# Optimization experiments

Measured on AMD Instinct MI355X. Metric: run time of the kernel, lower is better.

Reference implementation:

```python
import jax, jax.numpy as jnp
import numpy as np

N_NODES = 100000
N_EDGES = 1600000
N_GRAPHS = 250
F_NODE = 9
F_GLOB = 4
H = 64


def _lin(key, fan_out, fan_in):
    s = 1.0 / np.sqrt(fan_in)
    return jax.random.uniform(key, (fan_out, fan_in), jnp.float32, -s, s)


def setup_inputs() -> dict:
    key = jax.random.key(0)
    ks = jax.random.split(key, 24)
    inp = {
        "node_h": jax.random.normal(ks[0], (N_NODES, F_NODE), jnp.float32),
        "x_global_features": jax.random.normal(ks[1], (N_GRAPHS, F_GLOB), jnp.float32),
        "edge_index": jax.random.randint(ks[2], (2, N_EDGES), 0, N_NODES, jnp.int32),
        "batch_idx": jnp.sort(jax.random.randint(ks[3], (N_NODES,), 0, N_GRAPHS, jnp.int32)),
    }
    # SAGEConv params: lin_l (neighbor, with bias) and lin_r (root, no bias)
    dims = [(H, F_NODE + F_GLOB), (H, H), (H, H)]
    k = 4
    for i, (o, fi) in enumerate(dims):
        inp[f"sage{i}_Wl"] = _lin(ks[k], o, fi); k += 1
        inp[f"sage{i}_bl"] = jnp.zeros((o,), jnp.float32)
        inp[f"sage{i}_Wr"] = _lin(ks[k], o, fi); k += 1
    # MLP: 64->64->64->64->1
    mdims = [(H, H), (H, H), (H, H), (1, H)]
    for i, (o, fi) in enumerate(mdims):
        inp[f"mlp_W{i}"] = _lin(ks[k], o, fi); k += 1
        inp[f"mlp_b{i}"] = jnp.zeros((o,), jnp.float32)
    return inp


def _sage_conv(x, src, dst, Wl, bl, Wr):
    # mean aggregation of source features at destination nodes
    msg = x[src]                                             # [E, F]
    agg = jax.ops.segment_sum(msg, dst, num_segments=N_NODES)
    deg = jax.ops.segment_sum(jnp.ones((src.shape[0], 1), x.dtype), dst, num_segments=N_NODES)
    agg = agg / jnp.maximum(deg, 1.0)
    return agg @ Wl.T + bl + x @ Wr.T


def reference(node_h, x_global_features, edge_index, batch_idx,
              sage0_Wl, sage0_bl, sage0_Wr,
              sage1_Wl, sage1_bl, sage1_Wr,
              sage2_Wl, sage2_bl, sage2_Wr,
              mlp_W0, mlp_b0, mlp_W1, mlp_b1, mlp_W2, mlp_b2, mlp_W3, mlp_b3):
    src, dst = edge_index[0], edge_index[1]
    # concat per-node features with gathered global features
    x = jnp.concatenate([node_h, x_global_features[batch_idx]], axis=1)  # [N, 13]
    x = jax.nn.relu(_sage_conv(x, src, dst, sage0_Wl, sage0_bl, sage0_Wr))
    x = jax.nn.relu(_sage_conv(x, src, dst, sage1_Wl, sage1_bl, sage1_Wr))
    x = _sage_conv(x, src, dst, sage2_Wl, sage2_bl, sage2_Wr)            # [N, 64]
    # scatter_mean pooling over graphs
    summed = jax.ops.segment_sum(x, batch_idx, num_segments=N_GRAPHS)
    cnt = jax.ops.segment_sum(jnp.ones((x.shape[0], 1), x.dtype), batch_idx, num_segments=N_GRAPHS)
    pooled = summed / jnp.maximum(cnt, 1.0)                              # [G, 64]
    h = jax.nn.relu(pooled @ mlp_W0.T + mlp_b0)
    h = jax.nn.relu(h @ mlp_W1.T + mlp_b1)
    h = jax.nn.relu(h @ mlp_W2.T + mlp_b2)
    out = h @ mlp_W3.T + mlp_b3                                          # [G, 1]
    return out.reshape(-1)
```

## Files before the change

### kernel.cpp

```cpp
#include <hip/hip_runtime.h>
#include <hip/hip_bf16.h>

#define N_NODES 100000
#define N_EDGES 1600000
#define N_GRAPHS 250
#define NB 391
#define BCAP 6144
#define BIN_BLOCKS 250
#define EPB 6400

typedef __hip_bfloat16 bf16;

__device__ __forceinline__ void atomAddF(float* p, float v) {
  unsafeAtomicAdd(p, v);
}

__device__ __forceinline__ float b2f(unsigned short u) {
  union { unsigned int i; float f; } v; v.i = ((unsigned)u) << 16; return v.f;
}

__device__ __forceinline__ void accb(float4& a, ushort4 u) {
  a.x += b2f(u.x); a.y += b2f(u.y); a.z += b2f(u.z); a.w += b2f(u.w);
}

__device__ __forceinline__ float4 b2f4(ushort4 u) {
  return make_float4(b2f(u.x), b2f(u.y), b2f(u.z), b2f(u.w));
}

__device__ __forceinline__ float4 add4(float4 a, float4 b) {
  return make_float4(a.x + b.x, a.y + b.y, a.z + b.z, a.w + b.w);
}

__global__ void concat_kernel(const float* __restrict__ nh, const float* __restrict__ xg,
                              const int* __restrict__ batch, bf16* __restrict__ x0b) {
  int idx = blockIdx.x * blockDim.x + threadIdx.x;
  if (idx >= N_NODES * 16) return;
  int n = idx >> 4, j = idx & 15;
  float v;
  if (j < 9)       v = nh[n * 9 + j];
  else if (j < 13) v = xg[batch[n] * 4 + (j - 9)];
  else             v = 0.0f;
  x0b[idx] = __float2bfloat16(v);
}

__global__ __launch_bounds__(256) void bin_kernel(const int* __restrict__ src,
                                                  const int* __restrict__ dst,
                                                  int* __restrict__ gcnt,
                                                  int* __restrict__ binned) {
  __shared__ int hist[NB];
  __shared__ int base[NB];
  const int t = threadIdx.x;
  for (int i = t; i < NB; i += 256) hist[i] = 0;
  __syncthreads();
  const int e0 = blockIdx.x * EPB;
  int d[25];
#pragma unroll
  for (int k = 0; k < 25; ++k) {
    d[k] = dst[e0 + k * 256 + t];
    atomicAdd(&hist[d[k] >> 8], 1);
  }
  __syncthreads();
  for (int i = t; i < NB; i += 256) {
    base[i] = atomicAdd(&gcnt[i], hist[i]);
    hist[i] = 0;
  }
  __syncthreads();
#pragma unroll
  for (int k = 0; k < 25; ++k) {
    const int dd = d[k];
    const int b = dd >> 8;
    const int s = src[e0 + k * 256 + t];
    const int r = atomicAdd(&hist[b], 1);
    const int pos = base[b] + r;
    if (pos < BCAP) binned[b * BCAP + pos] = ((dd & 255) << 17) | s;
  }
}

__global__ __launch_bounds__(512) void bucketscan_kernel(const int* __restrict__ gcnt,
                                                         int* __restrict__ bbase,
                                                         int* __restrict__ rowptr) {
  __shared__ int sh[512];
  int t = threadIdx.x;
  int v = (t < NB) ? gcnt[t] : 0;
  sh[t] = v;
  __syncthreads();
  for (int off = 1; off < 512; off <<= 1) {
    int u = (t >= off) ? sh[t - off] : 0;
    __syncthreads();
    sh[t] += u;
    __syncthreads();
  }
  if (t < NB) bbase[t] = sh[t] - v;
  if (t == 0) rowptr[N_NODES] = N_EDGES;
}

__global__ __launch_bounds__(256) void sort_kernel(const int* __restrict__ gcnt,
                                                   const int* __restrict__ bbase,
                                                   const int* __restrict__ binned,
                                                   int* __restrict__ esorted,
                                                   int* __restrict__ rowptr,
                                                   float* __restrict__ inv) {
  __shared__ int cnt[256];
  __shared__ int cur[256];
  __shared__ int sh[256];
  const int b = blockIdx.x, t = threadIdx.x;
  const int count = min(gcnt[b], BCAP);
  const int ebase = bbase[b];
  const int* __restrict__ bin = binned + b * BCAP;
  cnt[t] = 0;
  __syncthreads();
  for (int i = t; i < count; i += 256) atomicAdd(&cnt[bin[i] >> 17], 1);
  __syncthreads();
  const int c = cnt[t];
  sh[t] = c;
  __syncthreads();
  for (int off = 1; off < 256; off <<= 1) {
    int u = (t >= off) ? sh[t - off] : 0;
    __syncthreads();
    sh[t] += u;
    __syncthreads();
  }
  const int p = sh[t] - c;
  cur[t] = p;
  const int node = b * 256 + t;
  if (node < N_NODES) {
    rowptr[node] = ebase + p;
    inv[node] = 1.0f / fmaxf((float)c, 1.0f);
  }
  __syncthreads();
  for (int i = t; i < count; i += 256) {
    const int v = bin[i];
    const int r = atomicAdd(&cur[v >> 17], 1);
    esorted[ebase + r] = v & 0x1FFFF;
  }
}

template <int F, bool RELU, bool OUTF32>
__launch_bounds__(512)
__global__ void sage_fused(const bf16* __restrict__ xb, const int* __restrict__ rowptr,
                           const int* __restrict__ esorted, const float* __restrict__ inv,
                           const float* __restrict__ Wl, const float* __restrict__ bl,
                           const float* __restrict__ Wr, int Fw,
                           float* __restrict__ outf, bf16* __restrict__ outb) {
  constexpr int ST = (F == 64) ? 64 : 20;
  constexpr int NT = 32;
  __shared__ float Wlt[F * 64];
  __shared__ float Wrt[F * 64];
  __shared__ float asld[NT * ST];
  __shared__ float xsld[NT * ST];
  for (int i = threadIdx.x; i < 64 * F; i += 512) {
    int h = i & 63, f = i >> 6;
    Wlt[f * 64 + h] = (f < Fw) ? Wl[h * Fw + f] : 0.0f;
    Wrt[f * 64 + h] = (f < Fw) ? Wr[h * Fw + f] : 0.0f;
  }
  __syncthreads();
  const int lane = threadIdx.x & 63;
  const int w = threadIdx.x >> 6;
  const int q = lane >> 4;
  const int c = lane & 15;
  const int slot = w * 4 + q;
  const float blv = bl[lane];
  const ushort4* xbu = (const ushort4*)xb;
  const int ntiles = N_NODES / NT;
  for (int tile = blockIdx.x; tile < ntiles; tile += gridDim.x) {
    const int n = tile * NT + slot;
    const int e0 = rowptr[n], e1 = rowptr[n + 1];
    const float invn = inv[n];
    if (F == 64) {
      float4 a0 = {0, 0, 0, 0}, a1 = a0, a2 = a0, a3 = a0;
      int e = e0;
      for (; e + 8 <= e1; e += 8) {
        int s0 = esorted[e], s1 = esorted[e + 1], s2 = esorted[e + 2], s3 = esorted[e + 3];
        int s4 = esorted[e + 4], s5 = esorted[e + 5], s6 = esorted[e + 6], s7 = esorted[e + 7];
        ushort4 u0 = xbu[(size_t)s0 * 16 + c];
        ushort4 u1 = xbu[(size_t)s1 * 16 + c];
        ushort4 u2 = xbu[(size_t)s2 * 16 + c];
        ushort4 u3 = xbu[(size_t)s3 * 16 + c];
        ushort4 u4 = xbu[(size_t)s4 * 16 + c];
        ushort4 u5 = xbu[(size_t)s5 * 16 + c];
        ushort4 u6 = xbu[(size_t)s6 * 16 + c];
        ushort4 u7 = xbu[(size_t)s7 * 16 + c];
        accb(a0, u0); accb(a1, u1); accb(a2, u2); accb(a3, u3);
        accb(a0, u4); accb(a1, u5); accb(a2, u6); accb(a3, u7);
      }
      for (; e + 4 <= e1; e += 4) {
        int s0 = esorted[e], s1 = esorted[e + 1], s2 = esorted[e + 2], s3 = esorted[e + 3];
        ushort4 u0 = xbu[(size_t)s0 * 16 + c];
        ushort4 u1 = xbu[(size_t)s1 * 16 + c];
        ushort4 u2 = xbu[(size_t)s2 * 16 + c];
        ushort4 u3 = xbu[(size_t)s3 * 16 + c];
        accb(a0, u0); accb(a1, u1); accb(a2, u2); accb(a3, u3);
      }
      for (; e < e1; ++e) accb(a0, xbu[(size_t)esorted[e] * 16 + c]);
      a0 = add4(add4(a0, a1), add4(a2, a3));
      float4 xv = b2f4(xbu[(size_t)n * 16 + c]);
      a0.x *= invn; a0.y *= invn; a0.z *= invn; a0.w *= invn;
      *(float4*)&asld[slot * ST + 4 * c] = a0;
      *(float4*)&xsld[slot * ST + 4 * c] = xv;
    } else {
      const int eg = c >> 2, cc = c & 3;
      float4 a0 = {0, 0, 0, 0}, a1 = a0;
      int e = e0 + eg;
      for (; e + 4 < e1; e += 8) {
        int sa = esorted[e], sb = esorted[e + 4];
        ushort4 ua = xbu[(size_t)sa * 4 + cc];
        ushort4 ub = xbu[(size_t)sb * 4 + cc];
        accb(a0, ua); accb(a1, ub);
      }
      if (e < e1) accb(a0, xbu[(size_t)esorted[e] * 4 + cc]);
      a0 = add4(a0, a1);
      a0.x += __shfl_xor(a0.x, 4); a0.y += __shfl_xor(a0.y, 4);
      a0.z += __shfl_xor(a0.z, 4); a0.w += __shfl_xor(a0.w, 4);
      a0.x += __shfl_xor(a0.x, 8); a0.y += __shfl_xor(a0.y, 8);
      a0.z += __shfl_xor(a0.z, 8); a0.w += __shfl_xor(a0.w, 8);
      if (eg == 0) {
        float4 xv = b2f4(xbu[(size_t)n * 4 + cc]);
        a0.x *= invn; a0.y *= invn; a0.z *= invn; a0.w *= invn;
        *(float4*)&asld[slot * ST + 4 * cc] = a0;
        *(float4*)&xsld[slot * ST + 4 * cc] = xv;
      }
    }
    __builtin_amdgcn_wave_barrier();
    const float* ar0 = &asld[(w * 4 + 0) * ST];
    const float* ar1 = &asld[(w * 4 + 1) * ST];
    const float* ar2 = &asld[(w * 4 + 2) * ST];
    const float* ar3 = &asld[(w * 4 + 3) * ST];
    const float* xr0 = &xsld[(w * 4 + 0) * ST];
    const float* xr1 = &xsld[(w * 4 + 1) * ST];
    const float* xr2 = &xsld[(w * 4 + 2) * ST];
    const float* xr3 = &xsld[(w * 4 + 3) * ST];
    float o0 = blv, o1 = blv, o2 = blv, o3 = blv;
#pragma unroll
    for (int f = 0; f < F; ++f) {
      float wl = Wlt[f * 64 + lane];
      float wr = Wrt[f * 64 + lane];
      o0 = fmaf(ar0[f], wl, fmaf(xr0[f], wr, o0));
      o1 = fmaf(ar1[f], wl, fmaf(xr1[f], wr, o1));
      o2 = fmaf(ar2[f], wl, fmaf(xr2[f], wr, o2));
      o3 = fmaf(ar3[f], wl, fmaf(xr3[f], wr, o3));
    }
    if (RELU) {
      o0 = fmaxf(o0, 0.0f); o1 = fmaxf(o1, 0.0f);
      o2 = fmaxf(o2, 0.0f); o3 = fmaxf(o3, 0.0f);
    }
    const size_t nb = (size_t)(tile * NT + w * 4) * 64;
    if (OUTF32) {
      outf[nb + lane]       = o0;
      outf[nb + 64 + lane]  = o1;
      outf[nb + 128 + lane] = o2;
      outf[nb + 192 + lane] = o3;
    } else {
      outb[nb + lane]       = __float2bfloat16(o0);
      outb[nb + 64 + lane]  = __float2bfloat16(o1);
      outb[nb + 128 + lane] = __float2bfloat16(o2);
      outb[nb + 192 + lane] = __float2bfloat16(o3);
    }
    __builtin_amdgcn_wave_barrier();
  }
}

__global__ void pool_kernel(const float* __restrict__ x, const int* __restrict__ batch,
                            float* __restrict__ pooled, float* __restrict__ cnt) {
  int wave = (blockIdx.x * blockDim.x + threadIdx.x) >> 6;
  int lane = threadIdx.x & 63;
  int n0 = wave * 64;
  if (n0 >= N_NODES) return;
  int nend = n0 + 64 < N_NODES ? n0 + 64 : N_NODES;
  int cur = -1;
  float acc = 0.0f, run = 0.0f;
  for (int n = n0; n < nend; ++n) {
    int b = batch[n];
    float v = x[(size_t)n * 64 + lane];
    if (b != cur) {
      if (cur >= 0) {
        atomAddF(&pooled[cur * 64 + lane], acc);
        if (lane == 0) atomAddF(&cnt[cur], run);
      }
      cur = b; acc = v; run = 1.0f;
    } else {
      acc += v; run += 1.0f;
    }
  }
  if (cur >= 0) {
    atomAddF(&pooled[cur * 64 + lane], acc);
    if (lane == 0) atomAddF(&cnt[cur], run);
  }
}

__global__ void mlp_kernel(const float* __restrict__ pooled, const float* __restrict__ cnt,
                           const float* __restrict__ W0, const float* __restrict__ b0,
                           const float* __restrict__ W1, const float* __restrict__ b1,
                           const float* __restrict__ W2, const float* __restrict__ b2,
                           const float* __restrict__ W3, const float* __restrict__ b3,
                           float* __restrict__ out) {
  int g = blockIdx.x, t = threadIdx.x;
  __shared__ float buf[2][64];
  float ic = 1.0f / fmaxf(cnt[g], 1.0f);
  buf[0][t] = pooled[g * 64 + t] * ic;
  __syncthreads();
  const float* Ws[3] = {W0, W1, W2};
  const float* Bs[3] = {b0, b1, b2};
  int cur = 0;
  for (int L = 0; L < 3; ++L) {
    const float* W = Ws[L];
    float acc = Bs[L][t];
#pragma unroll
    for (int f = 0; f < 64; ++f) acc = fmaf(W[t * 64 + f], buf[cur][f], acc);
    buf[cur ^ 1][t] = fmaxf(acc, 0.0f);
    __syncthreads();
    cur ^= 1;
  }
  float v = W3[t] * buf[cur][t];
  for (int off = 32; off; off >>= 1) v += __shfl_down(v, off);
  if (t == 0) out[g] = v + b3[0];
}

extern "C" void kernel_launch(void* const* d_in, const int* in_sizes, int n_in,
                              void* d_out, int out_size, void* d_ws, size_t ws_size,
                              hipStream_t stream) {
  const float* nh    = (const float*)d_in[0];
  const float* xg    = (const float*)d_in[1];
  const int*   ei    = (const int*)d_in[2];
  const int*   batch = (const int*)d_in[3];
  const float* s0Wl  = (const float*)d_in[4];
  const float* s0bl  = (const float*)d_in[5];
  const float* s0Wr  = (const float*)d_in[6];
  const float* s1Wl  = (const float*)d_in[7];
  const float* s1bl  = (const float*)d_in[8];
  const float* s1Wr  = (const float*)d_in[9];
  const float* s2Wl  = (const float*)d_in[10];
  const float* s2bl  = (const float*)d_in[11];
  const float* s2Wr  = (const float*)d_in[12];
  const float* mW0   = (const float*)d_in[13];
  const float* mb0   = (const float*)d_in[14];
  const float* mW1   = (const float*)d_in[15];
  const float* mb1   = (const float*)d_in[16];
  const float* mW2   = (const float*)d_in[17];
  const float* mb2   = (const float*)d_in[18];
  const float* mW3   = (const float*)d_in[19];
  const float* mb3   = (const float*)d_in[20];

  const int* src = ei;
  const int* dst = ei + N_EDGES;

  float* B0f    = (float*)d_ws;
  bf16*  x0b    = (bf16*)(B0f + (size_t)N_NODES * 64);
  bf16*  B0b    = (bf16*)((float*)x0b + (size_t)N_NODES * 8);
  bf16*  B1b    = (bf16*)((float*)B0b + (size_t)N_NODES * 32);
  float* inv    = (float*)B1b + (size_t)N_NODES * 32;
  float* pooled = inv + N_NODES;
  float* cnt    = pooled + (size_t)N_GRAPHS * 64;
  int*   rowptr  = (int*)(cnt + 256);
  int*   esorted = rowptr + 100004;
  int*   gcnt    = esorted + N_EDGES;
  int*   bbase   = gcnt + 400;
  int*   binned  = (int*)B1b;

  hipMemsetAsync(gcnt, 0, NB * sizeof(int), stream);
  hipMemsetAsync(pooled, 0, (N_GRAPHS * 64 + N_GRAPHS) * sizeof(float), stream);

  bin_kernel<<<BIN_BLOCKS, 256, 0, stream>>>(src, dst, gcnt, binned);
  bucketscan_kernel<<<1, 512, 0, stream>>>(gcnt, bbase, rowptr);
  sort_kernel<<<NB, 256, 0, stream>>>(gcnt, bbase, binned, esorted, rowptr, inv);

  concat_kernel<<<(N_NODES * 16 + 255) / 256, 256, 0, stream>>>(nh, xg, batch, x0b);

  sage_fused<16, true, false><<<1024, 512, 0, stream>>>(x0b, rowptr, esorted, inv,
                                                        s0Wl, s0bl, s0Wr, 13, nullptr, B0b);
  sage_fused<64, true, false><<<768, 512, 0, stream>>>(B0b, rowptr, esorted, inv,
                                                       s1Wl, s1bl, s1Wr, 64, nullptr, B1b);
  sage_fused<64, false, true><<<768, 512, 0, stream>>>(B1b, rowptr, esorted, inv,
                                                       s2Wl, s2bl, s2Wr, 64, B0f, nullptr);

  pool_kernel<<<((N_NODES + 63) / 64 * 64 + 255) / 256, 256, 0, stream>>>(B0f, batch, pooled, cnt);
  mlp_kernel<<<N_GRAPHS, 64, 0, stream>>>(pooled, cnt, mW0, mb0, mW1, mb1, mW2, mb2, mW3, mb3,
                                          (float*)d_out);
}
```

Measured before the change: 383.6 us.

## Split SAGE kernels and use 16-byte gathers with two edge groups for F=64 layers

The 64-feature SAGE layers move to a dedicated kernel with 1024-thread blocks and 64-node tiles. Each node is now served by 16 lanes, split into two edge-parity groups of 8 lanes, and each lane gathers a uint4 (8 bf16 values) per neighbor instead of a ushort4. This halves the number of gather instructions per edge and doubles edge-level parallelism per node; the two halves are combined with a cross-lane shuffle. The self-feature load is handled by the second group. The change adds tail guards for the non-divisible node count and a larger per-block LDS footprint, and the 16-feature first layer gets its own specialized kernel.

```diff
diff --git a/kernel.cpp b/kernel.cpp
--- a/kernel.cpp
+++ b/kernel.cpp
@@ -19,8 +19,19 @@
   union { unsigned int i; float f; } v; v.i = ((unsigned)u) << 16; return v.f;
 }
 
+__device__ __forceinline__ float asF(unsigned int i) {
+  union { unsigned int i; float f; } v; v.i = i; return v.f;
+}
+
 __device__ __forceinline__ void accb(float4& a, ushort4 u) {
   a.x += b2f(u.x); a.y += b2f(u.y); a.z += b2f(u.z); a.w += b2f(u.w);
+}
+
+__device__ __forceinline__ void acc8(float4& lo, float4& hi, uint4 u) {
+  lo.x += asF(u.x << 16); lo.y += asF(u.x & 0xffff0000u);
+  lo.z += asF(u.y << 16); lo.w += asF(u.y & 0xffff0000u);
+  hi.x += asF(u.z << 16); hi.y += asF(u.z & 0xffff0000u);
+  hi.z += asF(u.w << 16); hi.w += asF(u.w & 0xffff0000u);
 }
 
 __device__ __forceinline__ float4 b2f4(ushort4 u) {
@@ -135,15 +146,128 @@
   }
 }
 
-template <int F, bool RELU, bool OUTF32>
+template <bool RELU, bool OUTF32>
+__launch_bounds__(1024)
+__global__ void sage64_kernel(const bf16* __restrict__ xb, const int* __restrict__ rowptr,
+                              const int* __restrict__ esorted, const float* __restrict__ inv,
+                              const float* __restrict__ Wl, const float* __restrict__ bl,
+                              const float* __restrict__ Wr,
+                              float* __restrict__ outf, bf16* __restrict__ outb) {
+  constexpr int ST = 64;
+  constexpr int NT = 64;
+  __shared__ float Wlt[64 * 64];
+  __shared__ float Wrt[64 * 64];
+  __shared__ float asld[NT * ST];
+  __shared__ float xsld[NT * ST];
+  for (int i = threadIdx.x; i < 64 * 64; i += 1024) {
+    int h = i & 63, f = i >> 6;
+    Wlt[f * 64 + h] = Wl[h * 64 + f];
+    Wrt[f * 64 + h] = Wr[h * 64 + f];
+  }
+  __syncthreads();
+  const int lane = threadIdx.x & 63;
+  const int w = threadIdx.x >> 6;
+  const int q = lane >> 4;
+  const int g = (lane >> 3) & 1;
+  const int c = lane & 7;
+  const int slot = w * 4 + q;
+  const float blv = bl[lane];
+  const uint4* xb4 = (const uint4*)xb;
+  const int ntiles = (N_NODES + NT - 1) / NT;
+  for (int tile = blockIdx.x; tile < ntiles; tile += gridDim.x) {
+    const int n = tile * NT + slot;
+    const bool valid = n < N_NODES;
+    int e0 = 0, e1 = 0;
+    float invn = 0.0f;
+    uint4 uself = {0, 0, 0, 0};
+    if (valid) {
+      e0 = rowptr[n]; e1 = rowptr[n + 1]; invn = inv[n];
+      if (g) uself = xb4[(size_t)n * 8 + c];
+    }
+    float4 a0 = {0, 0, 0, 0}, a1 = a0, b0v = a0, b1v = a0;
+    int e = e0 + g;
+    for (; e + 6 < e1; e += 8) {
+      int s0 = esorted[e];
+      int s1 = esorted[e + 2];
+      int s2 = esorted[e + 4];
+      int s3 = esorted[e + 6];
+      uint4 u0 = xb4[(size_t)s0 * 8 + c];
+      uint4 u1 = xb4[(size_t)s1 * 8 + c];
+      uint4 u2 = xb4[(size_t)s2 * 8 + c];
+      uint4 u3 = xb4[(size_t)s3 * 8 + c];
+      acc8(a0, a1, u0); acc8(b0v, b1v, u1); acc8(a0, a1, u2); acc8(b0v, b1v, u3);
+    }
+    for (; e < e1; e += 2) {
+      uint4 u = xb4[(size_t)esorted[e] * 8 + c];
+      acc8(a0, a1, u);
+    }
+    a0 = add4(a0, b0v); a1 = add4(a1, b1v);
+    a0.x += __shfl_xor(a0.x, 8); a0.y += __shfl_xor(a0.y, 8);
+    a0.z += __shfl_xor(a0.z, 8); a0.w += __shfl_xor(a0.w, 8);
+    a1.x += __shfl_xor(a1.x, 8); a1.y += __shfl_xor(a1.y, 8);
+    a1.z += __shfl_xor(a1.z, 8); a1.w += __shfl_xor(a1.w, 8);
+    if (g == 0) {
+      a0.x *= invn; a0.y *= invn; a0.z *= invn; a0.w *= invn;
+      a1.x *= invn; a1.y *= invn; a1.z *= invn; a1.w *= invn;
+      *(float4*)&asld[slot * ST + 8 * c]     = a0;
+      *(float4*)&asld[slot * ST + 8 * c + 4] = a1;
+    } else {
+      float4 x0v, x1v;
+      x0v.x = asF(uself.x << 16); x0v.y = asF(uself.x & 0xffff0000u);
+      x0v.z = asF(uself.y << 16); x0v.w = asF(uself.y & 0xffff0000u);
+      x1v.x = asF(uself.z << 16); x1v.y = asF(uself.z & 0xffff0000u);
+      x1v.z = asF(uself.w << 16); x1v.w = asF(uself.w & 0xffff0000u);
+      *(float4*)&xsld[slot * ST + 8 * c]     = x0v;
+      *(float4*)&xsld[slot * ST + 8 * c + 4] = x1v;
+    }
+    __builtin_amdgcn_wave_barrier();
+    const float* ar0 = &asld[(w * 4 + 0) * ST];
+    const float* ar1 = &asld[(w * 4 + 1) * ST];
+    const float* ar2 = &asld[(w * 4 + 2) * ST];
+    const float* ar3 = &asld[(w * 4 + 3) * ST];
+    const float* xr0 = &xsld[(w * 4 + 0) * ST];
+    const float* xr1 = &xsld[(w * 4 + 1) * ST];
+    const float* xr2 = &xsld[(w * 4 + 2) * ST];
+    const float* xr3 = &xsld[(w * 4 + 3) * ST];
+    float o0 = blv, o1 = blv, o2 = blv, o3 = blv;
+#pragma unroll
+    for (int f = 0; f < 64; ++f) {
+      float wl = Wlt[f * 64 + lane];
+      float wr = Wrt[f * 64 + lane];
+      o0 = fmaf(ar0[f], wl, fmaf(xr0[f], wr, o0));
+      o1 = fmaf(ar1[f], wl, fmaf(xr1[f], wr, o1));
+      o2 = fmaf(ar2[f], wl, fmaf(xr2[f], wr, o2));
+      o3 = fmaf(ar3[f], wl, fmaf(xr3[f], wr, o3));
+    }
+    if (RELU) {
+      o0 = fmaxf(o0, 0.0f); o1 = fmaxf(o1, 0.0f);
+      o2 = fmaxf(o2, 0.0f); o3 = fmaxf(o3, 0.0f);
+    }
+    const int nbase = tile * NT + w * 4;
+    if (nbase < N_NODES) {
+      const size_t nb = (size_t)nbase * 64;
+      if (OUTF32) {
+        outf[nb + lane]       = o0;
+        outf[nb + 64 + lane]  = o1;
+        outf[nb + 128 + lane] = o2;
+        outf[nb + 192 + lane] = o3;
+      } else {
+        outb[nb + lane]       = __float2bfloat16(o0);
+        outb[nb + 64 + lane]  = __float2bfloat16(o1);
+        outb[nb + 128 + lane] = __float2bfloat16(o2);
+        outb[nb + 192 + lane] = __float2bfloat16(o3);
+      }
+    }
+    __builtin_amdgcn_wave_barrier();
+  }
+}
+
 __launch_bounds__(512)
-__global__ void sage_fused(const bf16* __restrict__ xb, const int* __restrict__ rowptr,
-                           const int* __restrict__ esorted, const float* __restrict__ inv,
-                           const float* __restrict__ Wl, const float* __restrict__ bl,
-                           const float* __restrict__ Wr, int Fw,
-                           float* __restrict__ outf, bf16* __restrict__ outb) {
-  constexpr int ST = (F == 64) ? 64 : 20;
-  constexpr int NT = 32;
+__global__ void sage16_kernel(const bf16* __restrict__ xb, const int* __restrict__ rowptr,
+                              const int* __restrict__ esorted, const float* __restrict__ inv,
+                              const float* __restrict__ Wl, const float* __restrict__ bl,
+                              const float* __restrict__ Wr, int Fw, bf16* __restrict__ outb) {
+  constexpr int F = 16, ST = 20, NT = 32;
   __shared__ float Wlt[F * 64];
   __shared__ float Wrt[F * 64];
   __shared__ float asld[NT * ST];
@@ -166,59 +290,26 @@
     const int n = tile * NT + slot;
     const int e0 = rowptr[n], e1 = rowptr[n + 1];
     const float invn = inv[n];
-    if (F == 64) {
-      float4 a0 = {0, 0, 0, 0}, a1 = a0, a2 = a0, a3 = a0;
-      int e = e0;
-      for (; e + 8 <= e1; e += 8) {
-        int s0 = esorted[e], s1 = esorted[e + 1], s2 = esorted[e + 2], s3 = esorted[e + 3];
-        int s4 = esorted[e + 4], s5 = esorted[e + 5], s6 = esorted[e + 6], s7 = esorted[e + 7];
-        ushort4 u0 = xbu[(size_t)s0 * 16 + c];
-        ushort4 u1 = xbu[(size_t)s1 * 16 + c];
-        ushort4 u2 = xbu[(size_t)s2 * 16 + c];
-        ushort4 u3 = xbu[(size_t)s3 * 16 + c];
-        ushort4 u4 = xbu[(size_t)s4 * 16 + c];
-        ushort4 u5 = xbu[(size_t)s5 * 16 + c];
-        ushort4 u6 = xbu[(size_t)s6 * 16 + c];
-        ushort4 u7 = xbu[(size_t)s7 * 16 + c];
-        accb(a0, u0); accb(a1, u1); accb(a2, u2); accb(a3, u3);
-        accb(a0, u4); accb(a1, u5); accb(a2, u6); accb(a3, u7);
-      }
-      for (; e + 4 <= e1; e += 4) {
-        int s0 = esorted[e], s1 = esorted[e + 1], s2 = esorted[e + 2], s3 = esorted[e + 3];
-        ushort4 u0 = xbu[(size_t)s0 * 16 + c];
-        ushort4 u1 = xbu[(size_t)s1 * 16 + c];
-        ushort4 u2 = xbu[(size_t)s2 * 16 + c];
-        ushort4 u3 = xbu[(size_t)s3 * 16 + c];
-        accb(a0, u0); accb(a1, u1); accb(a2, u2); accb(a3, u3);
-      }
-      for (; e < e1; ++e) accb(a0, xbu[(size_t)esorted[e] * 16 + c]);
-      a0 = add4(add4(a0, a1), add4(a2, a3));
-      float4 xv = b2f4(xbu[(size_t)n * 16 + c]);
+    const int eg = c >> 2, cc = c & 3;
+    float4 a0 = {0, 0, 0, 0}, a1 = a0;
+    int e = e0 + eg;
+    for (; e + 4 < e1; e += 8) {
+      int sa = esorted[e], sb = esorted[e + 4];
+      ushort4 ua = xbu[(size_t)sa * 4 + cc];
+      ushort4 ub = xbu[(size_t)sb * 4 + cc];
+      accb(a0, ua); accb(a1, ub);
+    }
+    if (e < e1) accb(a0, xbu[(size_t)esorted[e] * 4 + cc]);
+    a0 = add4(a0, a1);
+    a0.x += __shfl_xor(a0.x, 4); a0.y += __shfl_xor(a0.y, 4);
+    a0.z += __shfl_xor(a0.z, 4); a0.w += __shfl_xor(a0.w, 4);
+    a0.x += __shfl_xor(a0.x, 8); a0.y += __shfl_xor(a0.y, 8);
+    a0.z += __shfl_xor(a0.z, 8); a0.w += __shfl_xor(a0.w, 8);
+    if (eg == 0) {
+      float4 xv = b2f4(xbu[(size_t)n * 4 + cc]);
       a0.x *= invn; a0.y *= invn; a0.z *= invn; a0.w *= invn;
-      *(float4*)&asld[slot * ST + 4 * c] = a0;
-      *(float4*)&xsld[slot * ST + 4 * c] = xv;
-    } else {
-      const int eg = c >> 2, cc = c & 3;
-      float4 a0 = {0, 0, 0, 0}, a1 = a0;
-      int e = e0 + eg;
-      for (; e + 4 < e1; e += 8) {
-        int sa = esorted[e], sb = esorted[e + 4];
-        ushort4 ua = xbu[(size_t)sa * 4 + cc];
-        ushort4 ub = xbu[(size_t)sb * 4 + cc];
-        accb(a0, ua); accb(a1, ub);
-      }
-      if (e < e1) accb(a0, xbu[(size_t)esorted[e] * 4 + cc]);
-      a0 = add4(a0, a1);
-      a0.x += __shfl_xor(a0.x, 4); a0.y += __shfl_xor(a0.y, 4);
-      a0.z += __shfl_xor(a0.z, 4); a0.w += __shfl_xor(a0.w, 4);
-      a0.x += __shfl_xor(a0.x, 8); a0.y += __shfl_xor(a0.y, 8);
-      a0.z += __shfl_xor(a0.z, 8); a0.w += __shfl_xor(a0.w, 8);
-      if (eg == 0) {
-        float4 xv = b2f4(xbu[(size_t)n * 4 + cc]);
-        a0.x *= invn; a0.y *= invn; a0.z *= invn; a0.w *= invn;
-        *(float4*)&asld[slot * ST + 4 * cc] = a0;
-        *(float4*)&xsld[slot * ST + 4 * cc] = xv;
-      }
+      *(float4*)&asld[slot * ST + 4 * cc] = a0;
+      *(float4*)&xsld[slot * ST + 4 * cc] = xv;
     }
     __builtin_amdgcn_wave_barrier();
     const float* ar0 = &asld[(w * 4 + 0) * ST];
@@ -239,22 +330,13 @@
       o2 = fmaf(ar2[f], wl, fmaf(xr2[f], wr, o2));
       o3 = fmaf(ar3[f], wl, fmaf(xr3[f], wr, o3));
     }
-    if (RELU) {
-      o0 = fmaxf(o0, 0.0f); o1 = fmaxf(o1, 0.0f);
-      o2 = fmaxf(o2, 0.0f); o3 = fmaxf(o3, 0.0f);
-    }
+    o0 = fmaxf(o0, 0.0f); o1 = fmaxf(o1, 0.0f);
+    o2 = fmaxf(o2, 0.0f); o3 = fmaxf(o3, 0.0f);
     const size_t nb = (size_t)(tile * NT + w * 4) * 64;
-    if (OUTF32) {
-      outf[nb + lane]       = o0;
-      outf[nb + 64 + lane]  = o1;
-      outf[nb + 128 + lane] = o2;
-      outf[nb + 192 + lane] = o3;
-    } else {
-      outb[nb + lane]       = __float2bfloat16(o0);
-      outb[nb + 64 + lane]  = __float2bfloat16(o1);
-      outb[nb + 128 + lane] = __float2bfloat16(o2);
-      outb[nb + 192 + lane] = __float2bfloat16(o3);
-    }
+    outb[nb + lane]       = __float2bfloat16(o0);
+    outb[nb + 64 + lane]  = __float2bfloat16(o1);
+    outb[nb + 128 + lane] = __float2bfloat16(o2);
+    outb[nb + 192 + lane] = __float2bfloat16(o3);
     __builtin_amdgcn_wave_barrier();
   }
 }
@@ -365,12 +447,12 @@
 
   concat_kernel<<<(N_NODES * 16 + 255) / 256, 256, 0, stream>>>(nh, xg, batch, x0b);
 
-  sage_fused<16, true, false><<<1024, 512, 0, stream>>>(x0b, rowptr, esorted, inv,
-                                                        s0Wl, s0bl, s0Wr, 13, nullptr, B0b);
-  sage_fused<64, true, false><<<768, 512, 0, stream>>>(B0b, rowptr, esorted, inv,
-                                                       s1Wl, s1bl, s1Wr, 64, nullptr, B1b);
-  sage_fused<64, false, true><<<768, 512, 0, stream>>>(B1b, rowptr, esorted, inv,
-                                                       s2Wl, s2bl, s2Wr, 64, B0f, nullptr);
+  sage16_kernel<<<1024, 512, 0, stream>>>(x0b, rowptr, esorted, inv,
+                                          s0Wl, s0bl, s0Wr, 13, B0b);
+  sage64_kernel<true, false><<<512, 1024, 0, stream>>>(B0b, rowptr, esorted, inv,
+                                                       s1Wl, s1bl, s1Wr, nullptr, B1b);
+  sage64_kernel<false, true><<<512, 1024, 0, stream>>>(B1b, rowptr, esorted, inv,
+                                                       s2Wl, s2bl, s2Wr, B0f, nullptr);
 
   pool_kernel<<<((N_NODES + 63) / 64 * 64 + 255) / 256, 256, 0, stream>>>(B0f, batch, pooled, cnt);
   mlp_kernel<<<N_GRAPHS, 64, 0, stream>>>(pooled, cnt, mW0, mb0, mW1, mb1, mW2, mb2, mW3, mb3,
```

New measurement: 368.6 us. 1.04x faster.
